# Optimization experiments

Measured on AMD Instinct MI355X. Metric: run time of the kernel, lower is better.

The kernel has to match this reference:

```python
import jax, jax.numpy as jnp
import numpy as np

N_NODES = 100000
N_EDGES = 1600000
S_FEAT = 16   # static node features
D_FEAT = 8    # dynamic node features
E_FEAT = 4    # edge features
K = 2
EDGE_IN = E_FEAT + 2 * S_FEAT + 2 * D_FEAT  # 52
HIDDEN = 2 * D_FEAT                          # 16


def setup_inputs() -> dict:
    key = jax.random.key(0)
    ks = jax.random.split(key, 12)
    inp = {
        "x_s": jax.random.normal(ks[0], (N_NODES, S_FEAT), jnp.float32),
        "x_d": jax.random.normal(ks[1], (N_NODES, D_FEAT), jnp.float32),
        "edge_attr": jax.random.normal(ks[2], (N_EDGES, E_FEAT), jnp.float32),
        # edge MLP: Linear(EDGE_IN->HIDDEN) + ReLU + Linear(HIDDEN->D_FEAT)
        "W1": jax.random.normal(ks[3], (HIDDEN, EDGE_IN), jnp.float32) / np.sqrt(EDGE_IN),
        "b1": jnp.zeros((HIDDEN,), jnp.float32),
        "W2": jax.random.normal(ks[4], (D_FEAT, HIDDEN), jnp.float32) / np.sqrt(HIDDEN),
        "b2": jnp.zeros((D_FEAT,), jnp.float32),
        # K+1 = 3 filter matrices, Linear(D->D, bias=False): y = x @ W.T
        "Wf0": jax.random.normal(ks[5], (D_FEAT, D_FEAT), jnp.float32) / np.sqrt(D_FEAT),
        "Wf1": jax.random.normal(ks[6], (D_FEAT, D_FEAT), jnp.float32) / np.sqrt(D_FEAT),
        "Wf2": jax.random.normal(ks[7], (D_FEAT, D_FEAT), jnp.float32) / np.sqrt(D_FEAT),
        "edge_index": jax.random.randint(ks[8], (2, N_EDGES), 0, N_NODES, jnp.int64
                                         if jax.config.jax_enable_x64 else jnp.int32),
    }
    return inp


def _edge_mlp(e, W1, b1, W2, b2):
    h = jax.nn.relu(e @ W1.T + b1)
    return h @ W2.T + b2


def reference(x_s, x_d, edge_attr, W1, b1, W2, b2, Wf0, Wf1, Wf2, edge_index):
    row, col = edge_index[0], edge_index[1]
    num_nodes = x_d.shape[0]

    # s_ij depends only on static inputs (x_s, x_d, edge_attr), not on `out`,
    # so it is identical across the K steps; compute it once. The per-step
    # boolean edge mask is applied multiplicatively below, which matches the
    # torch masked-gather/scatter exactly (normalization is per-edge).
    e_ij = jnp.concatenate(
        [x_s[row], x_s[col], x_d[row], x_d[col], edge_attr], axis=1)  # [E, 52]
    s_ij = _edge_mlp(e_ij, W1, b1, W2, b2)                            # [E, D]
    nrm = jnp.linalg.norm(s_ij, axis=1, keepdims=True)
    s_ij = jnp.where(nrm > 0, s_ij / jnp.where(nrm > 0, nrm, 1.0), 0.0)

    filters = [Wf0, Wf1, Wf2]
    out = x_d @ filters[0].T
    for k in range(K):
        mask = out.sum(1) != 0                         # [N]
        edge_mask = (mask[row] | mask[col]).astype(out.dtype)  # [E]
        hydraulic_gradient = out[col] - out[row]       # [E, D]
        shift_sum = hydraulic_gradient * s_ij * edge_mask[:, None]
        scattered = jax.ops.segment_sum(shift_sum, col, num_segments=num_nodes)
        scattered = scattered @ filters[k + 1].T
        out = out + scattered
    return out
```

## Files before the change

### kernel.cpp

```cpp
#include <hip/hip_runtime.h>

#define S_FEAT 16
#define D_FEAT 8
#define E_FEAT 4
#define EDGE_IN 52
#define HIDDEN 16
#define SCAN_CHUNK 2048
#define NSUB 8

typedef unsigned int uint4v __attribute__((ext_vector_type(4)));

__device__ __forceinline__ void mlp_sij(
    const float* __restrict__ x_s, const float* __restrict__ x_d,
    const float* __restrict__ edge_attr,
    const float* __restrict__ W1, const float* __restrict__ b1,
    const float* __restrict__ W2, const float* __restrict__ b2,
    int row, int col, int e, float s[D_FEAT])
{
    float in[EDGE_IN];
    {
        const float4* p = (const float4*)(x_s + (size_t)row * S_FEAT);
#pragma unroll
        for (int q = 0; q < 4; ++q) {
            float4 v = p[q];
            in[q * 4 + 0] = v.x; in[q * 4 + 1] = v.y;
            in[q * 4 + 2] = v.z; in[q * 4 + 3] = v.w;
        }
    }
    {
        const float4* p = (const float4*)(x_s + (size_t)col * S_FEAT);
#pragma unroll
        for (int q = 0; q < 4; ++q) {
            float4 v = p[q];
            in[16 + q * 4 + 0] = v.x; in[16 + q * 4 + 1] = v.y;
            in[16 + q * 4 + 2] = v.z; in[16 + q * 4 + 3] = v.w;
        }
    }
    {
        const float4* p = (const float4*)(x_d + (size_t)row * D_FEAT);
#pragma unroll
        for (int q = 0; q < 2; ++q) {
            float4 v = p[q];
            in[32 + q * 4 + 0] = v.x; in[32 + q * 4 + 1] = v.y;
            in[32 + q * 4 + 2] = v.z; in[32 + q * 4 + 3] = v.w;
        }
    }
    {
        const float4* p = (const float4*)(x_d + (size_t)col * D_FEAT);
#pragma unroll
        for (int q = 0; q < 2; ++q) {
            float4 v = p[q];
            in[40 + q * 4 + 0] = v.x; in[40 + q * 4 + 1] = v.y;
            in[40 + q * 4 + 2] = v.z; in[40 + q * 4 + 3] = v.w;
        }
    }
    {
        float4 v = *(const float4*)(edge_attr + (size_t)e * E_FEAT);
        in[48] = v.x; in[49] = v.y; in[50] = v.z; in[51] = v.w;
    }

    float h[HIDDEN];
#pragma unroll
    for (int i = 0; i < HIDDEN; ++i) {
        float acc = b1[i];
#pragma unroll
        for (int j = 0; j < EDGE_IN; ++j)
            acc = fmaf(in[j], W1[i * EDGE_IN + j], acc);
        h[i] = acc > 0.f ? acc : 0.f;
    }

    float nrm2 = 0.f;
#pragma unroll
    for (int i = 0; i < D_FEAT; ++i) {
        float acc = b2[i];
#pragma unroll
        for (int j = 0; j < HIDDEN; ++j)
            acc = fmaf(h[j], W2[i * HIDDEN + j], acc);
        s[i] = acc;
        nrm2 = fmaf(acc, acc, nrm2);
    }
    float nrm = sqrtf(nrm2);
    float inv = nrm > 0.f ? 1.f / nrm : 0.f;
#pragma unroll
    for (int i = 0; i < D_FEAT; ++i) s[i] *= inv;
}

__device__ __forceinline__ uint4v pack_rec(const float s[8], int row)
{
    int q[8];
#pragma unroll
    for (int i = 0; i < 8; ++i) {
        float v = fminf(fmaxf(s[i] * 2047.f, -2047.f), 2047.f);
        q[i] = (int)rintf(v) & 0xFFF;
    }
    uint4v r;
    r[0] = (unsigned)(q[0] | (q[1] << 12) | (q[2] << 24));
    r[1] = (unsigned)((q[2] >> 8) | (q[3] << 4) | (q[4] << 16) | (q[5] << 28));
    r[2] = (unsigned)((q[5] >> 4) | (q[6] << 8) | (q[7] << 20));
    r[3] = (unsigned)row;
    return r;
}

__device__ __forceinline__ float rec_s(uint4v r, int f)
{
    int off = f * 12;
    unsigned lo = off < 32 ? r[0] : (off < 64 ? r[1] : r[2]);
    unsigned hi = off < 32 ? r[1] : (off < 64 ? r[2] : 0u);
    unsigned sh = (unsigned)off & 31u;
    unsigned long long both = ((unsigned long long)hi << 32) | lo;
    int q = ((int)((unsigned)(both >> sh) << 20)) >> 20;
    return (float)q * (1.f / 2047.f);
}

__global__ __launch_bounds__(256) void zero_counts_kernel(int* __restrict__ counts, int M)
{
    int i = blockIdx.x * blockDim.x + threadIdx.x;
    if (i < M) counts[i] = 0;
}

__global__ __launch_bounds__(256) void hist_kernel(
    const int* __restrict__ ei, int E, int N, int* __restrict__ counts8)
{
    int e = blockIdx.x * blockDim.x + threadIdx.x;
    if (e >= E) return;
    int col = ei[E + e];
    atomicAdd(&counts8[(threadIdx.x & (NSUB - 1)) * N + col], 1);
}

__global__ __launch_bounds__(256) void scan_local_kernel(
    const int* __restrict__ counts8, int* __restrict__ partial,
    int* __restrict__ blocksums, int N)
{
    __shared__ int sh[256];
    int b = blockIdx.x, t = threadIdx.x;
    int base = b * SCAN_CHUNK + t * 8;
    int v[8];
    int run = 0;
#pragma unroll
    for (int j = 0; j < 8; ++j) {
        int c = 0;
        if (base + j < N) {
#pragma unroll
            for (int s8 = 0; s8 < NSUB; ++s8)
                c += counts8[s8 * N + base + j];
        }
        v[j] = run;
        run += c;
    }
    sh[t] = run;
    __syncthreads();
#pragma unroll
    for (int st = 1; st < 256; st <<= 1) {
        int x = (t >= st) ? sh[t - st] : 0;
        __syncthreads();
        sh[t] += x;
        __syncthreads();
    }
    int excl = sh[t] - run;
    if (t == 255) blocksums[b] = sh[255];
#pragma unroll
    for (int j = 0; j < 8; ++j)
        if (base + j < N) partial[base + j] = excl + v[j];
}

__global__ void scan_blk_kernel(int* __restrict__ blocksums, int NB)
{
    if (threadIdx.x == 0) {
        int run = 0;
        for (int i = 0; i < NB; ++i) { int c = blocksums[i]; blocksums[i] = run; run += c; }
    }
}

__global__ __launch_bounds__(256) void scan_add_kernel(
    int* __restrict__ offsets, int* __restrict__ cursor,
    const int* __restrict__ blocksums, int N, int E)
{
    int i = blockIdx.x * blockDim.x + threadIdx.x;
    if (i < N) {
        int off = offsets[i] + blocksums[i / SCAN_CHUNK];
        offsets[i] = off;
        cursor[i]  = off;
    } else if (i == N) {
        offsets[N] = E;
    }
}

__global__ __launch_bounds__(256) void proj_kernel(
    const float* __restrict__ x_s, const float* __restrict__ x_d,
    const float* __restrict__ W1, const float* __restrict__ b1,
    float* __restrict__ PR, float* __restrict__ PC, int N)
{
    int n = blockIdx.x * blockDim.x + threadIdx.x;
    if (n >= N) return;
    float xs[S_FEAT], xd[D_FEAT];
    {
        const float4* p = (const float4*)(x_s + (size_t)n * S_FEAT);
#pragma unroll
        for (int q = 0; q < 4; ++q) {
            float4 v = p[q];
            xs[q * 4 + 0] = v.x; xs[q * 4 + 1] = v.y;
            xs[q * 4 + 2] = v.z; xs[q * 4 + 3] = v.w;
        }
        const float4* pd = (const float4*)(x_d + (size_t)n * D_FEAT);
        float4 a = pd[0], b = pd[1];
        xd[0] = a.x; xd[1] = a.y; xd[2] = a.z; xd[3] = a.w;
        xd[4] = b.x; xd[5] = b.y; xd[6] = b.z; xd[7] = b.w;
    }
    float pr[HIDDEN], pc[HIDDEN];
#pragma unroll
    for (int i = 0; i < HIDDEN; ++i) {
        const float* w = W1 + i * EDGE_IN;
        float a = b1[i], c = 0.f;
#pragma unroll
        for (int j = 0; j < S_FEAT; ++j) {
            a = fmaf(xs[j], w[j], a);
            c = fmaf(xs[j], w[16 + j], c);
        }
#pragma unroll
        for (int j = 0; j < D_FEAT; ++j) {
            a = fmaf(xd[j], w[32 + j], a);
            c = fmaf(xd[j], w[40 + j], c);
        }
        pr[i] = a; pc[i] = c;
    }
    float4* prp = (float4*)(PR + (size_t)n * HIDDEN);
    float4* pcp = (float4*)(PC + (size_t)n * HIDDEN);
#pragma unroll
    for (int q = 0; q < 4; ++q) {
        prp[q] = make_float4(pr[q * 4], pr[q * 4 + 1], pr[q * 4 + 2], pr[q * 4 + 3]);
        pcp[q] = make_float4(pc[q * 4], pc[q * 4 + 1], pc[q * 4 + 2], pc[q * 4 + 3]);
    }
}

__global__ __launch_bounds__(256) void mlp_scatter_proj_kernel(
    const float* __restrict__ PR, const float* __restrict__ PC,
    const float* __restrict__ edge_attr,
    const float* __restrict__ W1,
    const float* __restrict__ W2, const float* __restrict__ b2,
    const int* __restrict__ ei, int E,
    int* __restrict__ cursor, uint4v* __restrict__ recs)
{
    int e = blockIdx.x * blockDim.x + threadIdx.x;
    if (e >= E) return;
    int row = ei[e], col = ei[E + e];

    float pr[HIDDEN], pc[HIDDEN];
    {
        const float4* p = (const float4*)(PR + (size_t)row * HIDDEN);
        const float4* c = (const float4*)(PC + (size_t)col * HIDDEN);
#pragma unroll
        for (int q = 0; q < 4; ++q) {
            float4 a = p[q], b = c[q];
            pr[q * 4 + 0] = a.x; pr[q * 4 + 1] = a.y;
            pr[q * 4 + 2] = a.z; pr[q * 4 + 3] = a.w;
            pc[q * 4 + 0] = b.x; pc[q * 4 + 1] = b.y;
            pc[q * 4 + 2] = b.z; pc[q * 4 + 3] = b.w;
        }
    }
    float4 ea = *(const float4*)(edge_attr + (size_t)e * E_FEAT);

    float h[HIDDEN];
#pragma unroll
    for (int i = 0; i < HIDDEN; ++i) {
        const float* w = W1 + i * EDGE_IN + 48;
        float acc = pr[i] + pc[i];
        acc = fmaf(ea.x, w[0], acc);
        acc = fmaf(ea.y, w[1], acc);
        acc = fmaf(ea.z, w[2], acc);
        acc = fmaf(ea.w, w[3], acc);
        h[i] = acc > 0.f ? acc : 0.f;
    }

    float s[D_FEAT];
    float nrm2 = 0.f;
#pragma unroll
    for (int i = 0; i < D_FEAT; ++i) {
        float acc = b2[i];
#pragma unroll
        for (int j = 0; j < HIDDEN; ++j)
            acc = fmaf(h[j], W2[i * HIDDEN + j], acc);
        s[i] = acc;
        nrm2 = fmaf(acc, acc, nrm2);
    }
    float nrm = sqrtf(nrm2);
    float inv = nrm > 0.f ? 1.f / nrm : 0.f;
#pragma unroll
    for (int i = 0; i < D_FEAT; ++i) s[i] *= inv;

    uint4v rec = pack_rec(s, row);
    int pos = atomicAdd(&cursor[col], 1);
    __builtin_nontemporal_store(rec, recs + pos);
}

__global__ __launch_bounds__(256) void mlp_scatter_direct_kernel(
    const float* __restrict__ x_s, const float* __restrict__ x_d,
    const float* __restrict__ edge_attr,
    const float* __restrict__ W1, const float* __restrict__ b1,
    const float* __restrict__ W2, const float* __restrict__ b2,
    const int* __restrict__ ei, int E,
    int* __restrict__ cursor, uint4v* __restrict__ recs)
{
    int e = blockIdx.x * blockDim.x + threadIdx.x;
    if (e >= E) return;
    int row = ei[e], col = ei[E + e];
    float s[D_FEAT];
    mlp_sij(x_s, x_d, edge_attr, W1, b1, W2, b2, row, col, e, s);
    uint4v rec = pack_rec(s, row);
    int pos = atomicAdd(&cursor[col], 1);
    __builtin_nontemporal_store(rec, recs + pos);
}

__global__ __launch_bounds__(256) void node_init_kernel(
    const float* __restrict__ x_d, const float* __restrict__ Wf0,
    float* __restrict__ out, int N)
{
    int n = blockIdx.x * blockDim.x + threadIdx.x;
    if (n >= N) return;
    float xd[D_FEAT];
    {
        const float4* p = (const float4*)(x_d + (size_t)n * D_FEAT);
        float4 a = p[0], b = p[1];
        xd[0] = a.x; xd[1] = a.y; xd[2] = a.z; xd[3] = a.w;
        xd[4] = b.x; xd[5] = b.y; xd[6] = b.z; xd[7] = b.w;
    }
    float o[D_FEAT];
#pragma unroll
    for (int i = 0; i < D_FEAT; ++i) {
        float acc = 0.f;
#pragma unroll
        for (int j = 0; j < D_FEAT; ++j)
            acc = fmaf(xd[j], Wf0[i * D_FEAT + j], acc);
        o[i] = acc;
    }
    float4* op = (float4*)(out + (size_t)n * D_FEAT);
    op[0] = make_float4(o[0], o[1], o[2], o[3]);
    op[1] = make_float4(o[4], o[5], o[6], o[7]);
}

__global__ __launch_bounds__(256) void csr_step_kernel(
    const float* __restrict__ out_in, float* __restrict__ out_out,
    const int* __restrict__ offsets, const uint4v* __restrict__ recs,
    const float* __restrict__ Wf, int N)
{
    int lane = threadIdx.x & 63;
    int node = blockIdx.x * 4 + (threadIdx.x >> 6);
    if (node >= N) return;
    int e_sub = lane >> 3, f = lane & 7;
    int beg = offsets[node], end = offsets[node + 1];
    float outc = out_in[(size_t)node * 8 + f];
    float sc = outc;
    sc += __shfl_xor(sc, 1); sc += __shfl_xor(sc, 2); sc += __shfl_xor(sc, 4);
    bool mc = (sc != 0.f);
    float acc = 0.f;
    for (int base = beg; base < end; base += 8) {
        int e = base + e_sub;
        bool valid = e < end;
        uint4v rec = (uint4v)(0u);
        if (valid) rec = __builtin_nontemporal_load(recs + e);
        int row = (int)rec[3];
        float s = rec_s(rec, f);
        float outr = out_in[(size_t)row * 8 + f];
        float sr = outr;
        sr += __shfl_xor(sr, 1); sr += __shfl_xor(sr, 2); sr += __shfl_xor(sr, 4);
        bool m = mc || (sr != 0.f);
        acc += m ? (outc - outr) * s : 0.f;
    }
    acc += __shfl_xor(acc, 8);
    acc += __shfl_xor(acc, 16);
    acc += __shfl_xor(acc, 32);
    float upd = 0.f;
#pragma unroll
    for (int j = 0; j < 8; ++j) {
        float aj = __shfl(acc, (lane & ~7) | j);
        upd = fmaf(Wf[f * 8 + j], aj, upd);
    }
    if (e_sub == 0)
        out_out[(size_t)node * 8 + f] = outc + upd;
}

__global__ __launch_bounds__(256) void fb_node_init_kernel(
    const float* __restrict__ x_d, const float* __restrict__ Wf0,
    float* __restrict__ out, float* __restrict__ scattered, int N)
{
    int n = blockIdx.x * blockDim.x + threadIdx.x;
    if (n >= N) return;
    float xd[D_FEAT];
    const float4* p = (const float4*)(x_d + (size_t)n * D_FEAT);
    float4 a = p[0], b = p[1];
    xd[0] = a.x; xd[1] = a.y; xd[2] = a.z; xd[3] = a.w;
    xd[4] = b.x; xd[5] = b.y; xd[6] = b.z; xd[7] = b.w;
    float o[D_FEAT];
#pragma unroll
    for (int i = 0; i < D_FEAT; ++i) {
        float acc = 0.f;
#pragma unroll
        for (int j = 0; j < D_FEAT; ++j)
            acc = fmaf(xd[j], Wf0[i * D_FEAT + j], acc);
        o[i] = acc;
    }
    float4* op = (float4*)(out + (size_t)n * D_FEAT);
    op[0] = make_float4(o[0], o[1], o[2], o[3]);
    op[1] = make_float4(o[4], o[5], o[6], o[7]);
    float4* sp = (float4*)(scattered + (size_t)n * D_FEAT);
    sp[0] = make_float4(0.f, 0.f, 0.f, 0.f);
    sp[1] = make_float4(0.f, 0.f, 0.f, 0.f);
}

__global__ __launch_bounds__(256) void fb_edge_step_kernel(
    const float* __restrict__ x_s, const float* __restrict__ x_d,
    const float* __restrict__ edge_attr,
    const float* __restrict__ W1, const float* __restrict__ b1,
    const float* __restrict__ W2, const float* __restrict__ b2,
    const float* __restrict__ out,
    const int* __restrict__ ei, int E, float* __restrict__ scattered)
{
    int e = blockIdx.x * blockDim.x + threadIdx.x;
    if (e >= E) return;
    int row = ei[e], col = ei[E + e];
    const float4* pr = (const float4*)(out + (size_t)row * D_FEAT);
    const float4* pc = (const float4*)(out + (size_t)col * D_FEAT);
    float4 r0 = pr[0], r1 = pr[1], c0 = pc[0], c1 = pc[1];
    float srow = r0.x + r0.y + r0.z + r0.w + r1.x + r1.y + r1.z + r1.w;
    float scol = c0.x + c0.y + c0.z + c0.w + c1.x + c1.y + c1.z + c1.w;
    if (srow == 0.f && scol == 0.f) return;
    float s[D_FEAT];
    mlp_sij(x_s, x_d, edge_attr, W1, b1, W2, b2, row, col, e, s);
    float* dst = scattered + (size_t)col * D_FEAT;
    atomicAdd(dst + 0, (c0.x - r0.x) * s[0]);
    atomicAdd(dst + 1, (c0.y - r0.y) * s[1]);
    atomicAdd(dst + 2, (c0.z - r0.z) * s[2]);
    atomicAdd(dst + 3, (c0.w - r0.w) * s[3]);
    atomicAdd(dst + 4, (c1.x - r1.x) * s[4]);
    atomicAdd(dst + 5, (c1.y - r1.y) * s[5]);
    atomicAdd(dst + 6, (c1.z - r1.z) * s[6]);
    atomicAdd(dst + 7, (c1.w - r1.w) * s[7]);
}

__global__ __launch_bounds__(256) void fb_node_update_kernel(
    float* __restrict__ out, float* __restrict__ scattered,
    const float* __restrict__ Wf, int N)
{
    int n = blockIdx.x * blockDim.x + threadIdx.x;
    if (n >= N) return;
    float sc[D_FEAT];
    float4* sp = (float4*)(scattered + (size_t)n * D_FEAT);
    float4 a = sp[0], b = sp[1];
    sc[0] = a.x; sc[1] = a.y; sc[2] = a.z; sc[3] = a.w;
    sc[4] = b.x; sc[5] = b.y; sc[6] = b.z; sc[7] = b.w;
    sp[0] = make_float4(0.f, 0.f, 0.f, 0.f);
    sp[1] = make_float4(0.f, 0.f, 0.f, 0.f);
    float4* op = (float4*)(out + (size_t)n * D_FEAT);
    float4 o0 = op[0], o1 = op[1];
    float o[D_FEAT] = {o0.x, o0.y, o0.z, o0.w, o1.x, o1.y, o1.z, o1.w};
#pragma unroll
    for (int i = 0; i < D_FEAT; ++i) {
        float acc = 0.f;
#pragma unroll
        for (int j = 0; j < D_FEAT; ++j)
            acc = fmaf(sc[j], Wf[i * D_FEAT + j], acc);
        o[i] += acc;
    }
    op[0] = make_float4(o[0], o[1], o[2], o[3]);
    op[1] = make_float4(o[4], o[5], o[6], o[7]);
}

extern "C" void kernel_launch(void* const* d_in, const int* in_sizes, int n_in,
                              void* d_out, int out_size, void* d_ws, size_t ws_size,
                              hipStream_t stream) {
    const float* x_s       = (const float*)d_in[0];
    const float* x_d       = (const float*)d_in[1];
    const float* edge_attr = (const float*)d_in[2];
    const float* W1        = (const float*)d_in[3];
    const float* b1        = (const float*)d_in[4];
    const float* W2        = (const float*)d_in[5];
    const float* b2        = (const float*)d_in[6];
    const float* Wf[3]     = {(const float*)d_in[7], (const float*)d_in[8],
                              (const float*)d_in[9]};
    const int*   ei        = (const int*)d_in[10];

    const int N = in_sizes[1] / D_FEAT;
    const int E = in_sizes[10] / 2;

    float* out = (float*)d_out;

    size_t off = 0;
    auto carve = [&](size_t bytes) { size_t p = off; off = (off + bytes + 255) & ~255ULL; return p; };
    size_t o_counts  = carve((size_t)NSUB * N * 4);
    size_t o_offsets = carve((size_t)(N + 1) * 4);
    size_t o_cursor  = carve((size_t)(N + 1) * 4);
    size_t o_bsums   = carve(256 * 4);
    size_t o_bufA    = carve((size_t)N * D_FEAT * 4);
    size_t o_recs    = carve((size_t)E * 16);
    const size_t need_base = off;
    size_t o_PR      = carve((size_t)N * HIDDEN * 4);
    size_t o_PC      = carve((size_t)N * HIDDEN * 4);
    const size_t need_full = off;

    dim3 blk(256);
    dim3 gE((E + 255) / 256);
    dim3 gN((N + 255) / 256);

    if (ws_size >= need_base) {
        char* ws = (char*)d_ws;
        int*   counts8 = (int*)(ws + o_counts);
        int*   offsets = (int*)(ws + o_offsets);
        int*   cursor  = (int*)(ws + o_cursor);
        int*   bsums   = (int*)(ws + o_bsums);
        float* bufA    = (float*)(ws + o_bufA);
        uint4v* recs   = (uint4v*)(ws + o_recs);

        const int NB = (N + SCAN_CHUNK - 1) / SCAN_CHUNK;

        zero_counts_kernel<<<dim3((NSUB * N + 255) / 256), blk, 0, stream>>>(counts8, NSUB * N);
        hist_kernel<<<gE, blk, 0, stream>>>(ei, E, N, counts8);
        scan_local_kernel<<<dim3(NB), blk, 0, stream>>>(counts8, offsets, bsums, N);
        scan_blk_kernel<<<dim3(1), dim3(64), 0, stream>>>(bsums, NB);
        scan_add_kernel<<<dim3((N + 256) / 256), blk, 0, stream>>>(offsets, cursor, bsums, N, E);

        node_init_kernel<<<gN, blk, 0, stream>>>(x_d, Wf[0], out, N);

        if (ws_size >= need_full) {
            float* PR = (float*)(ws + o_PR);
            float* PC = (float*)(ws + o_PC);
            proj_kernel<<<gN, blk, 0, stream>>>(x_s, x_d, W1, b1, PR, PC, N);
            mlp_scatter_proj_kernel<<<gE, blk, 0, stream>>>(
                PR, PC, edge_attr, W1, W2, b2, ei, E, cursor, recs);
        } else {
            mlp_scatter_direct_kernel<<<gE, blk, 0, stream>>>(
                x_s, x_d, edge_attr, W1, b1, W2, b2, ei, E, cursor, recs);
        }

        dim3 gC((N + 3) / 4);
        csr_step_kernel<<<gC, blk, 0, stream>>>(out, bufA, offsets, recs, Wf[1], N);
        csr_step_kernel<<<gC, blk, 0, stream>>>(bufA, out, offsets, recs, Wf[2], N);
    } else {
        float* scattered = (float*)d_ws;
        fb_node_init_kernel<<<gN, blk, 0, stream>>>(x_d, Wf[0], out, scattered, N);
        for (int k = 0; k < 2; ++k) {
            fb_edge_step_kernel<<<gE, blk, 0, stream>>>(
                x_s, x_d, edge_attr, W1, b1, W2, b2, out, ei, E, scattered);
            fb_node_update_kernel<<<gN, blk, 0, stream>>>(out, scattered, Wf[k + 1], N);
        }
    }
}
```

Measured before the change: 386.5 us.

## Store node projections in fp16, fuse init into projection, precompute row sums

The per-node projections PR/PC are now stored as fp16, halving the bytes gathered per edge in the MLP/scatter kernel. The node-init step is fused into the projection kernel, and each node's feature row sum is precomputed so the CSR steps read one float for the mask instead of doing shuffle reductions. The block-sum scan now runs as a wave-parallel scan instead of a single thread. fp16 projections add rounding error to the edge MLP inputs.

```diff
diff --git a/kernel.cpp b/kernel.cpp
--- a/kernel.cpp
+++ b/kernel.cpp
@@ -1,4 +1,5 @@
 #include <hip/hip_runtime.h>
+#include <hip/hip_fp16.h>
 
 #define S_FEAT 16
 #define D_FEAT 8
@@ -112,6 +113,18 @@
     return (float)q * (1.f / 2047.f);
 }
 
+__device__ __forceinline__ void unpack8h(uint4v w, float* dst)
+{
+#pragma unroll
+    for (int i = 0; i < 4; ++i) {
+        unsigned u = w[i];
+        __half2 h;
+        h = *reinterpret_cast<__half2*>(&u);
+        float2 f = __half22float2(h);
+        dst[2 * i] = f.x; dst[2 * i + 1] = f.y;
+    }
+}
+
 __global__ __launch_bounds__(256) void zero_counts_kernel(int* __restrict__ counts, int M)
 {
     int i = blockIdx.x * blockDim.x + threadIdx.x;
@@ -163,11 +176,21 @@
         if (base + j < N) partial[base + j] = excl + v[j];
 }
 
-__global__ void scan_blk_kernel(int* __restrict__ blocksums, int NB)
-{
-    if (threadIdx.x == 0) {
-        int run = 0;
-        for (int i = 0; i < NB; ++i) { int c = blocksums[i]; blocksums[i] = run; run += c; }
+__global__ __launch_bounds__(64) void scan_blk_kernel(int* __restrict__ bs, int NB)
+{
+    int lane = threadIdx.x;
+    int carry = 0;
+    for (int base = 0; base < NB; base += 64) {
+        int i = base + lane;
+        int orig = (i < NB) ? bs[i] : 0;
+        int v = orig;
+#pragma unroll
+        for (int st = 1; st < 64; st <<= 1) {
+            int t = __shfl_up(v, st);
+            if (lane >= st) v += t;
+        }
+        if (i < NB) bs[i] = carry + v - orig;
+        carry += __shfl(v, 63);
     }
 }
 
@@ -185,10 +208,12 @@
     }
 }
 
-__global__ __launch_bounds__(256) void proj_kernel(
+__global__ __launch_bounds__(256) void proj_init_kernel(
     const float* __restrict__ x_s, const float* __restrict__ x_d,
     const float* __restrict__ W1, const float* __restrict__ b1,
-    float* __restrict__ PR, float* __restrict__ PC, int N)
+    const float* __restrict__ Wf0,
+    __half* __restrict__ PRh, __half* __restrict__ PCh,
+    float* __restrict__ out, float* __restrict__ S, int N)
 {
     int n = blockIdx.x * blockDim.x + threadIdx.x;
     if (n >= N) return;
@@ -206,7 +231,7 @@
         xd[0] = a.x; xd[1] = a.y; xd[2] = a.z; xd[3] = a.w;
         xd[4] = b.x; xd[5] = b.y; xd[6] = b.z; xd[7] = b.w;
     }
-    float pr[HIDDEN], pc[HIDDEN];
+    __half prh[HIDDEN], pch[HIDDEN];
 #pragma unroll
     for (int i = 0; i < HIDDEN; ++i) {
         const float* w = W1 + i * EDGE_IN;
@@ -221,19 +246,34 @@
             a = fmaf(xd[j], w[32 + j], a);
             c = fmaf(xd[j], w[40 + j], c);
         }
-        pr[i] = a; pc[i] = c;
-    }
-    float4* prp = (float4*)(PR + (size_t)n * HIDDEN);
-    float4* pcp = (float4*)(PC + (size_t)n * HIDDEN);
-#pragma unroll
-    for (int q = 0; q < 4; ++q) {
-        prp[q] = make_float4(pr[q * 4], pr[q * 4 + 1], pr[q * 4 + 2], pr[q * 4 + 3]);
-        pcp[q] = make_float4(pc[q * 4], pc[q * 4 + 1], pc[q * 4 + 2], pc[q * 4 + 3]);
-    }
+        prh[i] = __float2half_rn(a);
+        pch[i] = __float2half_rn(c);
+    }
+    {
+        uint4v* pr = (uint4v*)(PRh + (size_t)n * HIDDEN);
+        uint4v* pc = (uint4v*)(PCh + (size_t)n * HIDDEN);
+        pr[0] = *(uint4v*)&prh[0]; pr[1] = *(uint4v*)&prh[8];
+        pc[0] = *(uint4v*)&pch[0]; pc[1] = *(uint4v*)&pch[8];
+    }
+    float o[D_FEAT];
+    float rs = 0.f;
+#pragma unroll
+    for (int i = 0; i < D_FEAT; ++i) {
+        float acc = 0.f;
+#pragma unroll
+        for (int j = 0; j < D_FEAT; ++j)
+            acc = fmaf(xd[j], Wf0[i * D_FEAT + j], acc);
+        o[i] = acc;
+        rs += acc;
+    }
+    float4* op = (float4*)(out + (size_t)n * D_FEAT);
+    op[0] = make_float4(o[0], o[1], o[2], o[3]);
+    op[1] = make_float4(o[4], o[5], o[6], o[7]);
+    S[n] = rs;
 }
 
 __global__ __launch_bounds__(256) void mlp_scatter_proj_kernel(
-    const float* __restrict__ PR, const float* __restrict__ PC,
+    const __half* __restrict__ PRh, const __half* __restrict__ PCh,
     const float* __restrict__ edge_attr,
     const float* __restrict__ W1,
     const float* __restrict__ W2, const float* __restrict__ b2,
@@ -246,16 +286,11 @@
 
     float pr[HIDDEN], pc[HIDDEN];
     {
-        const float4* p = (const float4*)(PR + (size_t)row * HIDDEN);
-        const float4* c = (const float4*)(PC + (size_t)col * HIDDEN);
-#pragma unroll
-        for (int q = 0; q < 4; ++q) {
-            float4 a = p[q], b = c[q];
-            pr[q * 4 + 0] = a.x; pr[q * 4 + 1] = a.y;
-            pr[q * 4 + 2] = a.z; pr[q * 4 + 3] = a.w;
-            pc[q * 4 + 0] = b.x; pc[q * 4 + 1] = b.y;
-            pc[q * 4 + 2] = b.z; pc[q * 4 + 3] = b.w;
-        }
+        const uint4v* p = (const uint4v*)(PRh + (size_t)row * HIDDEN);
+        const uint4v* c = (const uint4v*)(PCh + (size_t)col * HIDDEN);
+        uint4v p0 = p[0], p1 = p[1], c0 = c[0], c1 = c[1];
+        unpack8h(p0, pr); unpack8h(p1, pr + 8);
+        unpack8h(c0, pc); unpack8h(c1, pc + 8);
     }
     float4 ea = *(const float4*)(edge_attr + (size_t)e * E_FEAT);
 
@@ -312,18 +347,17 @@
 
 __global__ __launch_bounds__(256) void node_init_kernel(
     const float* __restrict__ x_d, const float* __restrict__ Wf0,
-    float* __restrict__ out, int N)
+    float* __restrict__ out, float* __restrict__ S, int N)
 {
     int n = blockIdx.x * blockDim.x + threadIdx.x;
     if (n >= N) return;
     float xd[D_FEAT];
-    {
-        const float4* p = (const float4*)(x_d + (size_t)n * D_FEAT);
-        float4 a = p[0], b = p[1];
-        xd[0] = a.x; xd[1] = a.y; xd[2] = a.z; xd[3] = a.w;
-        xd[4] = b.x; xd[5] = b.y; xd[6] = b.z; xd[7] = b.w;
-    }
+    const float4* p = (const float4*)(x_d + (size_t)n * D_FEAT);
+    float4 a = p[0], b = p[1];
+    xd[0] = a.x; xd[1] = a.y; xd[2] = a.z; xd[3] = a.w;
+    xd[4] = b.x; xd[5] = b.y; xd[6] = b.z; xd[7] = b.w;
     float o[D_FEAT];
+    float rs = 0.f;
 #pragma unroll
     for (int i = 0; i < D_FEAT; ++i) {
         float acc = 0.f;
@@ -331,14 +365,17 @@
         for (int j = 0; j < D_FEAT; ++j)
             acc = fmaf(xd[j], Wf0[i * D_FEAT + j], acc);
         o[i] = acc;
+        rs += acc;
     }
     float4* op = (float4*)(out + (size_t)n * D_FEAT);
     op[0] = make_float4(o[0], o[1], o[2], o[3]);
     op[1] = make_float4(o[4], o[5], o[6], o[7]);
+    S[n] = rs;
 }
 
 __global__ __launch_bounds__(256) void csr_step_kernel(
     const float* __restrict__ out_in, float* __restrict__ out_out,
+    const float* __restrict__ S_in, float* __restrict__ S_out,
     const int* __restrict__ offsets, const uint4v* __restrict__ recs,
     const float* __restrict__ Wf, int N)
 {
@@ -348,9 +385,7 @@
     int e_sub = lane >> 3, f = lane & 7;
     int beg = offsets[node], end = offsets[node + 1];
     float outc = out_in[(size_t)node * 8 + f];
-    float sc = outc;
-    sc += __shfl_xor(sc, 1); sc += __shfl_xor(sc, 2); sc += __shfl_xor(sc, 4);
-    bool mc = (sc != 0.f);
+    bool mc = (S_in[node] != 0.f);
     float acc = 0.f;
     for (int base = beg; base < end; base += 8) {
         int e = base + e_sub;
@@ -360,9 +395,7 @@
         int row = (int)rec[3];
         float s = rec_s(rec, f);
         float outr = out_in[(size_t)row * 8 + f];
-        float sr = outr;
-        sr += __shfl_xor(sr, 1); sr += __shfl_xor(sr, 2); sr += __shfl_xor(sr, 4);
-        bool m = mc || (sr != 0.f);
+        bool m = mc || (S_in[row] != 0.f);
         acc += m ? (outc - outr) * s : 0.f;
     }
     acc += __shfl_xor(acc, 8);
@@ -374,8 +407,15 @@
         float aj = __shfl(acc, (lane & ~7) | j);
         upd = fmaf(Wf[f * 8 + j], aj, upd);
     }
-    if (e_sub == 0)
-        out_out[(size_t)node * 8 + f] = outc + upd;
+    float o = outc + upd;
+    float rs = o;
+    rs += __shfl_xor(rs, 1);
+    rs += __shfl_xor(rs, 2);
+    rs += __shfl_xor(rs, 4);
+    if (e_sub == 0) {
+        out_out[(size_t)node * 8 + f] = o;
+        if (f == 0) S_out[node] = rs;
+    }
 }
 
 __global__ __launch_bounds__(256) void fb_node_init_kernel(
@@ -490,10 +530,12 @@
     size_t o_cursor  = carve((size_t)(N + 1) * 4);
     size_t o_bsums   = carve(256 * 4);
     size_t o_bufA    = carve((size_t)N * D_FEAT * 4);
+    size_t o_SA      = carve((size_t)N * 4);
+    size_t o_SB      = carve((size_t)N * 4);
     size_t o_recs    = carve((size_t)E * 16);
     const size_t need_base = off;
-    size_t o_PR      = carve((size_t)N * HIDDEN * 4);
-    size_t o_PC      = carve((size_t)N * HIDDEN * 4);
+    size_t o_PR      = carve((size_t)N * HIDDEN * 2);
+    size_t o_PC      = carve((size_t)N * HIDDEN * 2);
     const size_t need_full = off;
 
     dim3 blk(256);
@@ -507,6 +549,8 @@
         int*   cursor  = (int*)(ws + o_cursor);
         int*   bsums   = (int*)(ws + o_bsums);
         float* bufA    = (float*)(ws + o_bufA);
+        float* SA      = (float*)(ws + o_SA);
+        float* SB      = (float*)(ws + o_SB);
         uint4v* recs   = (uint4v*)(ws + o_recs);
 
         const int NB = (N + SCAN_CHUNK - 1) / SCAN_CHUNK;
@@ -517,22 +561,22 @@
         scan_blk_kernel<<<dim3(1), dim3(64), 0, stream>>>(bsums, NB);
         scan_add_kernel<<<dim3((N + 256) / 256), blk, 0, stream>>>(offsets, cursor, bsums, N, E);
 
-        node_init_kernel<<<gN, blk, 0, stream>>>(x_d, Wf[0], out, N);
-
         if (ws_size >= need_full) {
-            float* PR = (float*)(ws + o_PR);
-            float* PC = (float*)(ws + o_PC);
-            proj_kernel<<<gN, blk, 0, stream>>>(x_s, x_d, W1, b1, PR, PC, N);
+            __half* PRh = (__half*)(ws + o_PR);
+            __half* PCh = (__half*)(ws + o_PC);
+            proj_init_kernel<<<gN, blk, 0, stream>>>(
+                x_s, x_d, W1, b1, Wf[0], PRh, PCh, out, SA, N);
             mlp_scatter_proj_kernel<<<gE, blk, 0, stream>>>(
-                PR, PC, edge_attr, W1, W2, b2, ei, E, cursor, recs);
+                PRh, PCh, edge_attr, W1, W2, b2, ei, E, cursor, recs);
         } else {
+            node_init_kernel<<<gN, blk, 0, stream>>>(x_d, Wf[0], out, SA, N);
             mlp_scatter_direct_kernel<<<gE, blk, 0, stream>>>(
                 x_s, x_d, edge_attr, W1, b1, W2, b2, ei, E, cursor, recs);
         }
 
         dim3 gC((N + 3) / 4);
-        csr_step_kernel<<<gC, blk, 0, stream>>>(out, bufA, offsets, recs, Wf[1], N);
-        csr_step_kernel<<<gC, blk, 0, stream>>>(bufA, out, offsets, recs, Wf[2], N);
+        csr_step_kernel<<<gC, blk, 0, stream>>>(out, bufA, SA, SB, offsets, recs, Wf[1], N);
+        csr_step_kernel<<<gC, blk, 0, stream>>>(bufA, out, SB, SA, offsets, recs, Wf[2], N);
     } else {
         float* scattered = (float*)d_ws;
         fb_node_init_kernel<<<gN, blk, 0, stream>>>(x_d, Wf[0], out, scattered, N);
```

New measurement: 366.6 us. -5.2%, faster.
